# Optimization experiments

Measured on AMD Instinct MI355X. Metric: run time of the kernel, lower is better.

The kernel has to match this reference:

```python
import jax, jax.numpy as jnp
import numpy as np

N = 50000      # nodes
E = 800000     # edges (before self-loops)
IN_DIM = 256
HID = 128
HEADS = 4
HEAD_D = HID // HEADS
LAYERS = 2
EPS = 1e-5
SLOPE = 0.2    # GATv2 leaky_relu negative slope (PyG default)


def setup_inputs() -> dict:
    key = jax.random.key(0)
    ks = jax.random.split(key, 8)
    x = jax.random.normal(ks[0], (N, IN_DIM), dtype=jnp.float32)
    edge_index = jax.random.randint(ks[1], (2, E), 0, N, dtype=jnp.int64)
    s_in = (2.0 / (IN_DIM + HID)) ** 0.5
    s_h = (2.0 / (HID + HID)) ** 0.5
    return {
        'x': x,
        'W_in': jax.random.normal(ks[2], (IN_DIM, HID), dtype=jnp.float32) * s_in,
        'b_in': jnp.zeros((HID,), jnp.float32),
        'ln_in_g': jnp.ones((HID,), jnp.float32),
        'ln_in_b': jnp.zeros((HID,), jnp.float32),
        'Wl': jax.random.normal(ks[3], (LAYERS, HID, HID), dtype=jnp.float32) * s_h,
        'Wr': jax.random.normal(ks[4], (LAYERS, HID, HID), dtype=jnp.float32) * s_h,
        'att': jax.random.normal(ks[5], (LAYERS, HEADS, HEAD_D), dtype=jnp.float32) * s_h,
        'ln_g': jnp.ones((LAYERS, HID), jnp.float32),
        'ln_b': jnp.zeros((LAYERS, HID), jnp.float32),
        'edge_index': edge_index,
    }


def layer_norm(h, g, b):
    mu = jnp.mean(h, axis=-1, keepdims=True)
    var = jnp.mean(jnp.square(h - mu), axis=-1, keepdims=True)
    return (h - mu) * jax.lax.rsqrt(var + EPS) * g + b


def gatv2_conv(h, src, dst, Wl, Wr, att):
    # h: [N, HID]; src/dst: [E'] (self-loops included)
    xl = (h @ Wl).reshape(N, HEADS, HEAD_D)   # source transform (also message)
    xr = (h @ Wr).reshape(N, HEADS, HEAD_D)   # target transform
    e = jax.nn.leaky_relu(xl[src] + xr[dst], SLOPE)          # [E', H, D]
    logits = jnp.einsum('ehd,hd->eh', e, att)                # [E', H]
    # segment softmax over incoming edges of each dst node
    m = jax.lax.stop_gradient(jax.ops.segment_max(logits, dst, num_segments=N))
    a = jnp.exp(logits - m[dst])
    z = jax.ops.segment_sum(a, dst, num_segments=N)
    alpha = a / z[dst]                                       # [E', H]
    out = jax.ops.segment_sum(xl[src] * alpha[:, :, None], dst, num_segments=N)
    return out.reshape(N, HID)


def reference(x, W_in, b_in, ln_in_g, ln_in_b, Wl, Wr, att, ln_g, ln_b, edge_index):
    loops = jnp.arange(N, dtype=edge_index.dtype)
    src = jnp.concatenate([edge_index[0], loops])
    dst = jnp.concatenate([edge_index[1], loops])
    h = jax.nn.relu(layer_norm(x @ W_in + b_in, ln_in_g, ln_in_b))
    for l in range(LAYERS):
        h_new = jax.nn.elu(layer_norm(gatv2_conv(h, src, dst, Wl[l], Wr[l], att[l]), ln_g[l], ln_b[l]))
        h = h + h_new
    return h
```

## Files before the change

kernel.cpp:

```cpp
#include <hip/hip_runtime.h>
#include <hip/hip_bf16.h>


#define NN 50000
#define EE 800000
#define EP (EE + NN)
#define IN_DIM 256
#define HID 128
#define SLOPE 0.2f
#define LN_EPS 1e-5f
#define NB 196
#define L2E 1.4426950408889634f

typedef short s8v __attribute__((ext_vector_type(8)));
typedef float f4v __attribute__((ext_vector_type(4)));

__device__ __forceinline__ float u2f(unsigned int u) {
    union { unsigned int i; float f; } c; c.i = u; return c.f;
}
__device__ __forceinline__ unsigned short f2bf(float f) {
    union { float f; unsigned int i; } c; c.f = f;
    unsigned int r = (c.i + 0x7fffu + ((c.i >> 16) & 1u)) >> 16;
    return (unsigned short)r;
}
__device__ __forceinline__ void unpack8(const uint4 raw, float* m) {
    m[0] = u2f(raw.x << 16); m[1] = u2f(raw.x & 0xffff0000u);
    m[2] = u2f(raw.y << 16); m[3] = u2f(raw.y & 0xffff0000u);
    m[4] = u2f(raw.z << 16); m[5] = u2f(raw.z & 0xffff0000u);
    m[6] = u2f(raw.w << 16); m[7] = u2f(raw.w & 0xffff0000u);
}
__device__ __forceinline__ float quad_sum(float v) {
    v += __int_as_float(__builtin_amdgcn_update_dpp(
            0, __float_as_int(v), 0xB1 , 0xF, 0xF, true));
    v += __int_as_float(__builtin_amdgcn_update_dpp(
            0, __float_as_int(v), 0x4E , 0xF, 0xF, true));
    return v;
}

__global__ void prep_weights(const float* __restrict__ Win,
                             const float* __restrict__ Wl,
                             const float* __restrict__ Wr,
                             float4* __restrict__ wp,
                             int* __restrict__ cnt) {
    const int sid = blockIdx.x * 256 + threadIdx.x;
    for (int i = sid; i < NN; i += 12288) cnt[i] = 0;

    const float* W;
    int slot;
    if (sid < 4096) { W = Win; slot = sid; }
    else {
        const int m = (sid - 4096) >> 11;
        slot = (sid - 4096) & 2047;
        W = (m == 0) ? Wl : (m == 1) ? Wr : (m == 2) ? (Wl + 16384) : (Wr + 16384);
    }
    const int n = slot & 127;
    const int kbase = (slot >> 9) * 32 + ((slot >> 7) & 3) * 8;
    unsigned short o[8];
#pragma unroll
    for (int j = 0; j < 8; j++) o[j] = f2bf(W[(size_t)(kbase + j) * 128 + n]);
    wp[sid] = *(const float4*)o;
}

__global__ __launch_bounds__(256) void gemm_in_mfma(
        const float* __restrict__ x,
        const float4* __restrict__ wp,
        const float* __restrict__ bin,
        const float* __restrict__ g,
        const float* __restrict__ bb,
        unsigned short* __restrict__ hb) {
    __shared__ s8v wlds[4096];
    const int tid = threadIdx.x;
    const int wv = tid >> 6, lane = tid & 63;
    const int l15 = lane & 15, kseg = lane >> 4;
    const int row0 = blockIdx.x * 64 + wv * 16;
    const int arow = row0 + l15;
    const int r = (arow < NN) ? arow : 0;

    s8v afrag[8];
#pragma unroll
    for (int ks = 0; ks < 8; ks++) {
        const float* ap = x + (size_t)r * IN_DIM + ks * 32 + kseg * 8;
        const float4 a0 = *(const float4*)ap;
        const float4 a1 = *(const float4*)(ap + 4);
        unsigned short t[8] = { f2bf(a0.x), f2bf(a0.y), f2bf(a0.z), f2bf(a0.w),
                                f2bf(a1.x), f2bf(a1.y), f2bf(a1.z), f2bf(a1.w) };
        afrag[ks] = *(const s8v*)t;
    }

#pragma unroll
    for (int i = 0; i < 16; i++) {
        const int idx = i * 256 + tid;
        ((float4*)wlds)[idx] = wp[idx];
    }
    __syncthreads();

    f4v acc[8];
#pragma unroll
    for (int nb = 0; nb < 8; nb++) acc[nb] = (f4v){0.f, 0.f, 0.f, 0.f};
#pragma unroll
    for (int ks = 0; ks < 8; ks++) {
#pragma unroll
        for (int nb = 0; nb < 8; nb++) {
            const s8v bfrag = wlds[(ks * 4 + kseg) * 128 + nb * 16 + l15];
            acc[nb] = __builtin_amdgcn_mfma_f32_16x16x32_bf16(afrag[ks], bfrag, acc[nb], 0, 0, 0);
        }
    }

    float binv[8], gv[8], bbv[8];
#pragma unroll
    for (int nb = 0; nb < 8; nb++) {
        const int col = nb * 16 + l15;
        binv[nb] = bin[col]; gv[nb] = g[col]; bbv[nb] = bb[col];
    }
    float s1[4] = {0.f, 0.f, 0.f, 0.f}, s2[4] = {0.f, 0.f, 0.f, 0.f};
#pragma unroll
    for (int nb = 0; nb < 8; nb++)
#pragma unroll
        for (int reg = 0; reg < 4; reg++) {
            const float t = acc[nb][reg] + binv[nb];
            acc[nb][reg] = t;
            s1[reg] += t; s2[reg] += t * t;
        }
#pragma unroll
    for (int off = 1; off < 16; off <<= 1)
#pragma unroll
        for (int reg = 0; reg < 4; reg++) {
            s1[reg] += __shfl_xor(s1[reg], off);
            s2[reg] += __shfl_xor(s2[reg], off);
        }
    float mu[4], rstd[4];
#pragma unroll
    for (int reg = 0; reg < 4; reg++) {
        mu[reg] = s1[reg] / (float)HID;
        rstd[reg] = rsqrtf(s2[reg] / (float)HID - mu[reg] * mu[reg] + LN_EPS);
    }
    const int rbase = row0 + 4 * kseg;
#pragma unroll
    for (int reg = 0; reg < 4; reg++) {
        const int grow = rbase + reg;
        if (grow >= NN) continue;
#pragma unroll
        for (int nb = 0; nb < 8; nb++) {
            const int col = nb * 16 + l15;
            float v = (acc[nb][reg] - mu[reg]) * rstd[reg] * gv[nb] + bbv[nb];
            hb[(size_t)grow * HID + col] = f2bf(fmaxf(v, 0.f));
        }
    }
}

__global__ __launch_bounds__(256) void gemm_xlxr_mfma(
        const unsigned short* __restrict__ hb,
        const float4* __restrict__ wp,
        unsigned short* __restrict__ xl,
        unsigned short* __restrict__ xrb) {
    __shared__ s8v wlds[4096];
    const int tid = threadIdx.x;
    const int wv = tid >> 6, lane = tid & 63;
    const int l15 = lane & 15, kseg = lane >> 4;
    const int row0 = blockIdx.x * 64 + wv * 16;
    const int arow = row0 + l15;
    const int r = (arow < NN) ? arow : 0;

    s8v afrag[4];
#pragma unroll
    for (int ks = 0; ks < 4; ks++)
        afrag[ks] = *(const s8v*)(hb + (size_t)r * HID + ks * 32 + kseg * 8);

#pragma unroll
    for (int i = 0; i < 16; i++) {
        const int idx = i * 256 + tid;
        ((float4*)wlds)[idx] = wp[idx];
    }
    __syncthreads();

    f4v accL[8], accR[8];
#pragma unroll
    for (int nb = 0; nb < 8; nb++) {
        accL[nb] = (f4v){0.f, 0.f, 0.f, 0.f};
        accR[nb] = (f4v){0.f, 0.f, 0.f, 0.f};
    }
#pragma unroll
    for (int ks = 0; ks < 4; ks++) {
#pragma unroll
        for (int nb = 0; nb < 8; nb++) {
            const s8v bL = wlds[(ks * 4 + kseg) * 128 + nb * 16 + l15];
            accL[nb] = __builtin_amdgcn_mfma_f32_16x16x32_bf16(afrag[ks], bL, accL[nb], 0, 0, 0);
            const s8v bR = wlds[2048 + (ks * 4 + kseg) * 128 + nb * 16 + l15];
            accR[nb] = __builtin_amdgcn_mfma_f32_16x16x32_bf16(afrag[ks], bR, accR[nb], 0, 0, 0);
        }
    }

    const int rbase = row0 + 4 * kseg;
#pragma unroll
    for (int reg = 0; reg < 4; reg++) {
        const int grow = rbase + reg;
        if (grow >= NN) continue;
#pragma unroll
        for (int nb = 0; nb < 8; nb++) {
            const int col = nb * 16 + l15;
            xl[(size_t)grow * HID + col]  = f2bf(accL[nb][reg]);
            xrb[(size_t)grow * HID + col] = f2bf(accR[nb][reg]);
        }
    }
}

__global__ void dst_hist(const int* __restrict__ ei, int* __restrict__ cnt,
                         unsigned short* __restrict__ epos) {
    const long e = (long)blockIdx.x * 256 + threadIdx.x;
    if (e >= EP) return;
    const int d = (e < EE) ? ei[EE + e] : (int)(e - EE);
    epos[e] = (unsigned short)atomicAdd(&cnt[d], 1);
}

__global__ void scan_bsum(const int* __restrict__ cnt, int* __restrict__ bsum) {
    const int tid = threadIdx.x;
    const int i = blockIdx.x * 256 + tid;
    int v = (i < NN) ? cnt[i] : 0;
#pragma unroll
    for (int off = 1; off < 64; off <<= 1) v += __shfl_xor(v, off);
    __shared__ int ws[4];
    if ((tid & 63) == 0) ws[tid >> 6] = v;
    __syncthreads();
    if (tid == 0) bsum[blockIdx.x] = ws[0] + ws[1] + ws[2] + ws[3];
}

__global__ void scan_rowptr(const int* __restrict__ cnt,
                            const int* __restrict__ bsum,
                            int* __restrict__ rowptr) {
    const int tid = threadIdx.x;
    const int lane = tid & 63, wv = tid >> 6;
    __shared__ int ws[4];
    __shared__ int pref;

    {
        int v = (tid < blockIdx.x && tid < NB) ? bsum[tid] : 0;
#pragma unroll
        for (int off = 1; off < 64; off <<= 1) v += __shfl_xor(v, off);
        if (lane == 0) ws[wv] = v;
        __syncthreads();
        if (tid == 0) pref = ws[0] + ws[1] + ws[2] + ws[3];
        __syncthreads();
    }

    const int i = blockIdx.x * 256 + tid;
    const int v = (i < NN) ? cnt[i] : 0;
    int s = v;
#pragma unroll
    for (int off = 1; off < 64; off <<= 1) {
        const int u = __shfl_up(s, off);
        if (lane >= off) s += u;
    }
    __shared__ int wt[4];
    if (lane == 63) wt[wv] = s;
    __syncthreads();
    int add = pref;
    for (int w = 0; w < wv; w++) add += wt[w];
    const int excl = s + add - v;
    if (i < NN) rowptr[i] = excl;
    if (i == NN - 1) rowptr[NN] = excl + v;
}

__global__ void csr_scatter(const int* __restrict__ ei,
                            const int* __restrict__ rowptr,
                            const unsigned short* __restrict__ epos,
                            int* __restrict__ esrcb) {
    const long e = (long)blockIdx.x * 256 + threadIdx.x;
    if (e >= EP) return;
    int s, d;
    if (e < EE) { s = ei[e]; d = ei[EE + e]; }
    else        { s = d = (int)(e - EE); }
    esrcb[rowptr[d] + epos[e]] = s * (HID * 2);
}

__global__ __launch_bounds__(256) void gat_ln(
        const unsigned short* __restrict__ xl,
        const unsigned short* __restrict__ xrb,
        const float* __restrict__ att,
        const int* __restrict__ rowptr,
        const int* __restrict__ esrcb,
        const float* __restrict__ g,
        const float* __restrict__ b,
        const unsigned short* __restrict__ hres,
        float* __restrict__ dest,
        unsigned short* __restrict__ destb) {
    const int tid = threadIdx.x;
    const int lane = tid & 63;
    const int wv = tid >> 6;
    const int l16 = lane & 15;
    const int node = blockIdx.x * 16 + wv * 4 + (lane >> 4);
    const int f0 = l16 * 8;

    float xrv[8], a06[8], a04[8];
    {
        const uint4 xraw = *(const uint4*)(xrb + (size_t)node * HID + f0);
        unpack8(xraw, xrv);
        const float4 t0 = *(const float4*)(att + f0);
        const float4 t1 = *(const float4*)(att + f0 + 4);
        float av[8] = { t0.x, t0.y, t0.z, t0.w, t1.x, t1.y, t1.z, t1.w };
#pragma unroll
        for (int j = 0; j < 8; j++) {
            a06[j] = 0.6f * L2E * av[j];
            a04[j] = 0.4f * L2E * av[j];
        }
    }
    float gv[8], bv[8], hv[8];
    {
        const float4 g0 = *(const float4*)(g + f0);
        const float4 g1 = *(const float4*)(g + f0 + 4);
        gv[0]=g0.x; gv[1]=g0.y; gv[2]=g0.z; gv[3]=g0.w;
        gv[4]=g1.x; gv[5]=g1.y; gv[6]=g1.z; gv[7]=g1.w;
        const float4 b0 = *(const float4*)(b + f0);
        const float4 b1 = *(const float4*)(b + f0 + 4);
        bv[0]=b0.x; bv[1]=b0.y; bv[2]=b0.z; bv[3]=b0.w;
        bv[4]=b1.x; bv[5]=b1.y; bv[6]=b1.z; bv[7]=b1.w;
        const uint4 hraw = *(const uint4*)(hres + (size_t)node * HID + f0);
        unpack8(hraw, hv);
    }
    const int beg = rowptr[node];
    const int deg = rowptr[node + 1] - beg;
    int dmax = deg;
    dmax = max(dmax, __shfl_xor(dmax, 16));
    dmax = max(dmax, __shfl_xor(dmax, 32));

    const char* xlbase = (const char*)xl + f0 * 2;
    const int gb = lane & 48;

    float acc[8];
#pragma unroll
    for (int j = 0; j < 8; j++) acc[j] = 0.f;
    float z = 0.f;

    int sb_cur = (l16 < deg)      ? esrcb[beg + l16]      : 0;
    int sb_nxt = (16 + l16 < deg) ? esrcb[beg + 16 + l16] : 0;

#define PROCR(RAW, VALID) do {                                              \
        float m[8];                                                         \
        unpack8((RAW), m);                                                  \
        float v = 0.f;                                                      \
        _Pragma("unroll")                                                   \
        for (int j = 0; j < 8; j++) {                                       \
            const float tt = m[j] + xrv[j];                                 \
            v += tt * a06[j] + fabsf(tt) * a04[j];                          \
        }                                                                   \
        v = quad_sum(v);                           \
        const float a = (VALID) ? __builtin_amdgcn_exp2f(v) : 0.f;          \
        z += a;                                                             \
        _Pragma("unroll")                                                   \
        for (int j = 0; j < 8; j++) acc[j] = fmaf(a, m[j], acc[j]);         \
    } while (0)

    for (int t = 0; t < dmax; t += 4) {
        if ((t & 15) == 0 && t) {
            sb_cur = sb_nxt;
            sb_nxt = (t + 16 + l16 < deg) ? esrcb[beg + t + 16 + l16] : 0;
        }
        const int o0 = __shfl(sb_cur, gb | ((t + 0) & 15));
        const int o1 = __shfl(sb_cur, gb | ((t + 1) & 15));
        const int o2 = __shfl(sb_cur, gb | ((t + 2) & 15));
        const int o3 = __shfl(sb_cur, gb | ((t + 3) & 15));
        const uint4 r0 = *(const uint4*)(xlbase + o0);
        const uint4 r1 = *(const uint4*)(xlbase + o1);
        const uint4 r2 = *(const uint4*)(xlbase + o2);
        const uint4 r3 = *(const uint4*)(xlbase + o3);
        PROCR(r0, t + 0 < deg);
        PROCR(r1, t + 1 < deg);
        PROCR(r2, t + 2 < deg);
        PROCR(r3, t + 3 < deg);
    }
#undef PROCR

    const float inv = 1.f / z;
    float o[8];
    float s1 = 0.f, s2 = 0.f;
#pragma unroll
    for (int j = 0; j < 8; j++) {
        o[j] = acc[j] * inv;
        s1 += o[j];
        s2 = fmaf(o[j], o[j], s2);
    }
#pragma unroll
    for (int off = 1; off < 16; off <<= 1) {
        s1 += __shfl_xor(s1, off);
        s2 += __shfl_xor(s2, off);
    }
    const float mu = s1 / (float)HID;
    const float rstd = rsqrtf(s2 / (float)HID - mu * mu + LN_EPS);

    float res[8];
#pragma unroll
    for (int j = 0; j < 8; j++) {
        float n = (o[j] - mu) * rstd * gv[j] + bv[j];
        n = (n > 0.f) ? n : (__builtin_amdgcn_exp2f(n * L2E) - 1.f);
        res[j] = hv[j] + n;
    }
    if (dest) {
        float* dp = dest + (size_t)node * HID + f0;
        *(float4*)dp       = (float4){res[0], res[1], res[2], res[3]};
        *(float4*)(dp + 4) = (float4){res[4], res[5], res[6], res[7]};
    }
    if (destb) {
        unsigned short o16[8];
#pragma unroll
        for (int j = 0; j < 8; j++) o16[j] = f2bf(res[j]);
        *(uint4*)(destb + (size_t)node * HID + f0) = *(const uint4*)o16;
    }
}

extern "C" void kernel_launch(void* const* d_in, const int* in_sizes, int n_in,
                              void* d_out, int out_size, void* d_ws, size_t ws_size,
                              hipStream_t stream) {
    const float* x       = (const float*)d_in[0];
    const float* W_in    = (const float*)d_in[1];
    const float* b_in    = (const float*)d_in[2];
    const float* ln_in_g = (const float*)d_in[3];
    const float* ln_in_b = (const float*)d_in[4];
    const float* Wl      = (const float*)d_in[5];
    const float* Wr      = (const float*)d_in[6];
    const float* att     = (const float*)d_in[7];
    const float* ln_g    = (const float*)d_in[8];
    const float* ln_b    = (const float*)d_in[9];
    const int*   ei      = (const int*)d_in[10];
    float* out = (float*)d_out;

    unsigned short* hb  = (unsigned short*)d_ws;
    unsigned short* hb2 = hb  + (size_t)NN * HID;
    unsigned short* xlb = hb2 + (size_t)NN * HID;
    unsigned short* xrb = xlb + (size_t)NN * HID;
    float4* wp = (float4*)(xrb + (size_t)NN * HID);
    int* cnt    = (int*)(wp + 12288);
    int* rowptr = cnt + NN;
    int* bsum   = rowptr + (NN + 1);
    int* esrcb  = bsum + NB;
    unsigned short* epos = (unsigned short*)(esrcb + EP);

    prep_weights<<<48, 256, 0, stream>>>(W_in, Wl, Wr, wp, cnt);

    const int eblocks = (EP + 255) / 256;
    dst_hist<<<eblocks, 256, 0, stream>>>(ei, cnt, epos);
    scan_bsum<<<NB, 256, 0, stream>>>(cnt, bsum);
    scan_rowptr<<<NB, 256, 0, stream>>>(cnt, bsum, rowptr);
    csr_scatter<<<eblocks, 256, 0, stream>>>(ei, rowptr, epos, esrcb);

    const int mblocks = (NN + 63) / 64;
    gemm_in_mfma<<<mblocks, 256, 0, stream>>>(x, wp, b_in, ln_in_g, ln_in_b, hb);

    for (int l = 0; l < 2; l++) {
        const unsigned short* hsrc = (l == 0) ? hb : hb2;
        gemm_xlxr_mfma<<<mblocks, 256, 0, stream>>>(hsrc, wp + 4096 + l * 4096, xlb, xrb);
        gat_ln<<<NN / 16, 256, 0, stream>>>(xlb, xrb, att + (size_t)l * HID,
                                            rowptr, esrcb,
                                            ln_g + (size_t)l * HID,
                                            ln_b + (size_t)l * HID,
                                            hsrc,
                                            (l == 1) ? out : (float*)nullptr,
                                            (l == 0) ? hb2 : (unsigned short*)nullptr);
    }
}
```

Before: 183.1 us.

## Fuse CSR build phases into one cooperative kernel with grid syncs

Replaces the four separate CSR-construction kernels (histogram, block sums, row-pointer scan, scatter) and the count zeroing with a single cooperative kernel of 512 blocks that separates the phases with grid-wide syncs. This removes several kernel launches and their inter-kernel gaps on the stream. The trade-off is grid-stride loops over fewer blocks for the edge-parallel phases, plus the cost of each grid.sync.

```diff
diff --git a/kernel.cpp b/kernel.cpp
--- a/kernel.cpp
+++ b/kernel.cpp
@@ -1,5 +1,8 @@
 #include <hip/hip_runtime.h>
 #include <hip/hip_bf16.h>
+#include <hip/hip_cooperative_groups.h>
+
+namespace cg = cooperative_groups;
 
 
 #define NN 50000
@@ -10,6 +13,7 @@
 #define SLOPE 0.2f
 #define LN_EPS 1e-5f
 #define NB 196
+#define CSRB 512
 #define L2E 1.4426950408889634f
 
 typedef short s8v __attribute__((ext_vector_type(8)));
@@ -40,11 +44,8 @@
 __global__ void prep_weights(const float* __restrict__ Win,
                              const float* __restrict__ Wl,
                              const float* __restrict__ Wr,
-                             float4* __restrict__ wp,
-                             int* __restrict__ cnt) {
+                             float4* __restrict__ wp) {
     const int sid = blockIdx.x * 256 + threadIdx.x;
-    for (int i = sid; i < NN; i += 12288) cnt[i] = 0;
-
     const float* W;
     int slot;
     if (sid < 4096) { W = Win; slot = sid; }
@@ -59,6 +60,78 @@
 #pragma unroll
     for (int j = 0; j < 8; j++) o[j] = f2bf(W[(size_t)(kbase + j) * 128 + n]);
     wp[sid] = *(const float4*)o;
+}
+
+__global__ void csr_build(const int* __restrict__ ei,
+                          int* __restrict__ cnt,
+                          unsigned short* __restrict__ epos,
+                          int* __restrict__ bsum,
+                          int* __restrict__ rowptr,
+                          int* __restrict__ esrcb) {
+    cg::grid_group grid = cg::this_grid();
+    const int tid = threadIdx.x;
+    const int gtid = blockIdx.x * 256 + tid;
+    const int gstride = CSRB * 256;
+    const int lane = tid & 63, wv = tid >> 6;
+
+    for (int i = gtid; i < NN; i += gstride) cnt[i] = 0;
+    grid.sync();
+
+    for (int e = gtid; e < EP; e += gstride) {
+        const int d = (e < EE) ? ei[EE + e] : (e - EE);
+        epos[e] = (unsigned short)atomicAdd(&cnt[d], 1);
+    }
+    grid.sync();
+
+    if (blockIdx.x < NB) {
+        const int i = blockIdx.x * 256 + tid;
+        int v = (i < NN) ? cnt[i] : 0;
+#pragma unroll
+        for (int off = 1; off < 64; off <<= 1) v += __shfl_xor(v, off);
+        __shared__ int ws0[4];
+        if (lane == 0) ws0[wv] = v;
+        __syncthreads();
+        if (tid == 0) bsum[blockIdx.x] = ws0[0] + ws0[1] + ws0[2] + ws0[3];
+    }
+    grid.sync();
+
+    if (blockIdx.x < NB) {
+        __shared__ int ws[4];
+        __shared__ int pref;
+        {
+            int v = (tid < (int)blockIdx.x && tid < NB) ? bsum[tid] : 0;
+#pragma unroll
+            for (int off = 1; off < 64; off <<= 1) v += __shfl_xor(v, off);
+            if (lane == 0) ws[wv] = v;
+            __syncthreads();
+            if (tid == 0) pref = ws[0] + ws[1] + ws[2] + ws[3];
+            __syncthreads();
+        }
+        const int i = blockIdx.x * 256 + tid;
+        const int v = (i < NN) ? cnt[i] : 0;
+        int s = v;
+#pragma unroll
+        for (int off = 1; off < 64; off <<= 1) {
+            const int u = __shfl_up(s, off);
+            if (lane >= off) s += u;
+        }
+        __shared__ int wt[4];
+        if (lane == 63) wt[wv] = s;
+        __syncthreads();
+        int add = pref;
+        for (int w = 0; w < wv; w++) add += wt[w];
+        const int excl = s + add - v;
+        if (i < NN) rowptr[i] = excl;
+        if (i == NN - 1) rowptr[NN] = excl + v;
+    }
+    grid.sync();
+
+    for (int e = gtid; e < EP; e += gstride) {
+        int s, d;
+        if (e < EE) { s = ei[e]; d = ei[EE + e]; }
+        else        { s = d = e - EE; }
+        esrcb[rowptr[d] + epos[e]] = s * (HID * 2);
+    }
 }
 
 __global__ __launch_bounds__(256) void gemm_in_mfma(
@@ -202,74 +275,6 @@
             xrb[(size_t)grow * HID + col] = f2bf(accR[nb][reg]);
         }
     }
-}
-
-__global__ void dst_hist(const int* __restrict__ ei, int* __restrict__ cnt,
-                         unsigned short* __restrict__ epos) {
-    const long e = (long)blockIdx.x * 256 + threadIdx.x;
-    if (e >= EP) return;
-    const int d = (e < EE) ? ei[EE + e] : (int)(e - EE);
-    epos[e] = (unsigned short)atomicAdd(&cnt[d], 1);
-}
-
-__global__ void scan_bsum(const int* __restrict__ cnt, int* __restrict__ bsum) {
-    const int tid = threadIdx.x;
-    const int i = blockIdx.x * 256 + tid;
-    int v = (i < NN) ? cnt[i] : 0;
-#pragma unroll
-    for (int off = 1; off < 64; off <<= 1) v += __shfl_xor(v, off);
-    __shared__ int ws[4];
-    if ((tid & 63) == 0) ws[tid >> 6] = v;
-    __syncthreads();
-    if (tid == 0) bsum[blockIdx.x] = ws[0] + ws[1] + ws[2] + ws[3];
-}
-
-__global__ void scan_rowptr(const int* __restrict__ cnt,
-                            const int* __restrict__ bsum,
-                            int* __restrict__ rowptr) {
-    const int tid = threadIdx.x;
-    const int lane = tid & 63, wv = tid >> 6;
-    __shared__ int ws[4];
-    __shared__ int pref;
-
-    {
-        int v = (tid < blockIdx.x && tid < NB) ? bsum[tid] : 0;
-#pragma unroll
-        for (int off = 1; off < 64; off <<= 1) v += __shfl_xor(v, off);
-        if (lane == 0) ws[wv] = v;
-        __syncthreads();
-        if (tid == 0) pref = ws[0] + ws[1] + ws[2] + ws[3];
-        __syncthreads();
-    }
-
-    const int i = blockIdx.x * 256 + tid;
-    const int v = (i < NN) ? cnt[i] : 0;
-    int s = v;
-#pragma unroll
-    for (int off = 1; off < 64; off <<= 1) {
-        const int u = __shfl_up(s, off);
-        if (lane >= off) s += u;
-    }
-    __shared__ int wt[4];
-    if (lane == 63) wt[wv] = s;
-    __syncthreads();
-    int add = pref;
-    for (int w = 0; w < wv; w++) add += wt[w];
-    const int excl = s + add - v;
-    if (i < NN) rowptr[i] = excl;
-    if (i == NN - 1) rowptr[NN] = excl + v;
-}
-
-__global__ void csr_scatter(const int* __restrict__ ei,
-                            const int* __restrict__ rowptr,
-                            const unsigned short* __restrict__ epos,
-                            int* __restrict__ esrcb) {
-    const long e = (long)blockIdx.x * 256 + threadIdx.x;
-    if (e >= EP) return;
-    int s, d;
-    if (e < EE) { s = ei[e]; d = ei[EE + e]; }
-    else        { s = d = (int)(e - EE); }
-    esrcb[rowptr[d] + epos[e]] = s * (HID * 2);
 }
 
 __global__ __launch_bounds__(256) void gat_ln(
@@ -433,13 +438,14 @@
     int* esrcb  = bsum + NB;
     unsigned short* epos = (unsigned short*)(esrcb + EP);
 
-    prep_weights<<<48, 256, 0, stream>>>(W_in, Wl, Wr, wp, cnt);
-
-    const int eblocks = (EP + 255) / 256;
-    dst_hist<<<eblocks, 256, 0, stream>>>(ei, cnt, epos);
-    scan_bsum<<<NB, 256, 0, stream>>>(cnt, bsum);
-    scan_rowptr<<<NB, 256, 0, stream>>>(cnt, bsum, rowptr);
-    csr_scatter<<<eblocks, 256, 0, stream>>>(ei, rowptr, epos, esrcb);
+    prep_weights<<<48, 256, 0, stream>>>(W_in, Wl, Wr, wp);
+
+    {
+        void* args[] = { (void*)&ei, (void*)&cnt, (void*)&epos,
+                         (void*)&bsum, (void*)&rowptr, (void*)&esrcb };
+        (void)hipLaunchCooperativeKernel((void*)csr_build, dim3(CSRB), dim3(256),
+                                         args, 0, stream);
+    }
 
     const int mblocks = (NN + 63) / 64;
     gemm_in_mfma<<<mblocks, 256, 0, stream>>>(x, wp, b_in, ln_in_g, ln_in_b, hb);
```

Result: slower. 384.8 us (+110.2%).
